# Performance work log

Hardware: AMD Instinct MI355X
Metric: run time of the kernel (lower is better)

The kernel has to match this reference:

```python
import jax, jax.numpy as jnp
import numpy as np

N_NODES = 100000
N_EDGES = 2000000
N_GRAPHS = 2000
IN_DIM = 7
EDGE_DIM = 4
HID = 32
N_CLASSES = 2
NEG_SLOPE = 0.2
BN_EPS = 1e-5


def setup_inputs() -> dict:
    key = jax.random.key(0)
    ks = jax.random.split(key, 16)
    x = jax.random.normal(ks[0], (N_NODES, IN_DIM), dtype=jnp.float32)
    edge_index = jax.random.randint(ks[1], (2, N_EDGES), 0, N_NODES, dtype=jnp.int64)
    batch = jnp.sort(jax.random.randint(ks[2], (N_NODES,), 0, N_GRAPHS, dtype=jnp.int64))
    edge_attr = jax.random.normal(ks[3], (N_EDGES, EDGE_DIM), dtype=jnp.float32)
    s = 0.1
    W0 = jax.random.normal(ks[4], (IN_DIM, HID), dtype=jnp.float32) * s
    W12 = jax.random.normal(ks[5], (2, HID, HID), dtype=jnp.float32) * s
    att_src = jax.random.normal(ks[6], (3, HID), dtype=jnp.float32) * s
    att_dst = jax.random.normal(ks[7], (3, HID), dtype=jnp.float32) * s
    lin_edge = jax.random.normal(ks[8], (3, EDGE_DIM, HID), dtype=jnp.float32) * s
    att_edge = jax.random.normal(ks[9], (3, HID), dtype=jnp.float32) * s
    bias = jnp.zeros((3, HID), dtype=jnp.float32)
    bn_gamma = jnp.ones((3, HID), dtype=jnp.float32)
    bn_beta = jnp.zeros((3, HID), dtype=jnp.float32)
    fc_W = jax.random.normal(ks[10], (HID, N_CLASSES), dtype=jnp.float32) * s
    fc_b = jnp.zeros((N_CLASSES,), dtype=jnp.float32)
    return dict(x=x, edge_index=edge_index, batch=batch, edge_attr=edge_attr,
                W0=W0, W12=W12, att_src=att_src, att_dst=att_dst,
                lin_edge=lin_edge, att_edge=att_edge, bias=bias,
                bn_gamma=bn_gamma, bn_beta=bn_beta, fc_W=fc_W, fc_b=fc_b)


def gat_layer(x, src, dst, edge_attr, W, a_src, a_dst, We, a_edge, b):
    # PyG GATConv, heads=1, add_self_loops=False: edge_attr conditions attention only.
    N = x.shape[0]
    h = x @ W                                   # [N, H]
    e = edge_attr @ We                          # [E, H]
    score = ((h * a_src).sum(-1)[src]
             + (h * a_dst).sum(-1)[dst]
             + (e * a_edge).sum(-1))            # [E]
    score = jax.nn.leaky_relu(score, NEG_SLOPE)
    m = jax.ops.segment_max(score, dst, num_segments=N)
    w = jnp.exp(score - m[dst])
    denom = jax.ops.segment_sum(w, dst, num_segments=N)
    alpha = w / (denom[dst] + 1e-16)            # segment softmax over incoming edges
    out = jax.ops.segment_sum(h[src] * alpha[:, None], dst, num_segments=N)
    return out + b


def batchnorm(x, gamma, beta):
    mu = x.mean(axis=0)
    var = ((x - mu) ** 2).mean(axis=0)          # biased var, as torch BN normalization
    return (x - mu) * jax.lax.rsqrt(var + BN_EPS) * gamma + beta


def reference(x, edge_index, batch, edge_attr, W0, W12, att_src, att_dst,
              lin_edge, att_edge, bias, bn_gamma, bn_beta, fc_W, fc_b):
    src, dst = edge_index[0], edge_index[1]
    Ws = [W0, W12[0], W12[1]]
    h = x
    for l in range(3):
        h = gat_layer(h, src, dst, edge_attr, Ws[l], att_src[l], att_dst[l],
                      lin_edge[l], att_edge[l], bias[l])
        h = batchnorm(h, bn_gamma[l], bn_beta[l])
        h = jax.nn.relu(h)
    node_embs = h
    graph_emb = jax.ops.segment_sum(node_embs, batch, num_segments=N_GRAPHS)
    out = graph_emb @ fc_W + fc_b
    return (out, node_embs, graph_emb)
```

## Files before the change

kernel.cpp:

```cpp
#include <hip/hip_runtime.h>
#include <hip/hip_bf16.h>
#include <math.h>

#define N_NODES   100000
#define N_EDGES   2000000
#define N_GRAPHS  2000
#define IN_DIM    7
#define EDGE_DIM  4
#define HID       32
#define N_CLASSES 2
#define NEG_SLOPE 0.2f
#define BN_EPS    1e-5f
#define SCAN_B    1024

__global__ void k_ce_all(const float* __restrict__ lin_edge, const float* __restrict__ att_edge,
                         float* __restrict__ ce3, float* __restrict__ gsum3,
                         float* __restrict__ gsq3) {
    int t = threadIdx.x;
    if (t < 12) {
        int l = t >> 2, d = t & 3;
        float s = 0.f;
        for (int k = 0; k < HID; ++k)
            s += lin_edge[(size_t)l * EDGE_DIM * HID + d * HID + k] * att_edge[l * HID + k];
        ce3[t] = s;
    }
    if (t < 3 * HID) { gsum3[t] = 0.f; gsq3[t] = 0.f; }
}

__global__ void k_hist(const int* __restrict__ dst, int* __restrict__ deg) {
    int e = blockIdx.x * blockDim.x + threadIdx.x;
    if (e < N_EDGES) atomicAdd(deg + dst[e], 1);
}

__global__ void k_scan1(const int* __restrict__ deg, int* __restrict__ offs,
                        int* __restrict__ bsum) {
    __shared__ int wsum[16];
    int t = threadIdx.x, lane = t & 63, w = t >> 6;
    int i = blockIdx.x * SCAN_B + t;
    int v = (i < N_NODES) ? deg[i] : 0;
    int x = v;
#pragma unroll
    for (int o = 1; o < 64; o <<= 1) { int y = __shfl_up(x, o, 64); if (lane >= o) x += y; }
    if (lane == 63) wsum[w] = x;
    __syncthreads();
    if (t < 16) {
        int s = wsum[t];
#pragma unroll
        for (int o = 1; o < 16; o <<= 1) { int y = __shfl_up(s, o, 16); if (t >= o) s += y; }
        wsum[t] = s;
    }
    __syncthreads();
    int excl = (w ? wsum[w - 1] : 0) + x - v;
    if (i < N_NODES) offs[i] = excl;
    if (t == 0) bsum[blockIdx.x] = wsum[15];
}

__global__ void k_scan2(int* __restrict__ bsum, int nb) {
    __shared__ int w0;
    int t = threadIdx.x, lane = t & 63, w = t >> 6;
    int v = (t < nb) ? bsum[t] : 0;
    int x = v;
#pragma unroll
    for (int o = 1; o < 64; o <<= 1) { int y = __shfl_up(x, o, 64); if (lane >= o) x += y; }
    if (w == 0 && lane == 63) w0 = x;
    __syncthreads();
    int excl = x - v + (w ? w0 : 0);
    if (t < nb) bsum[t] = excl;
}

__global__ void k_scan3(int* __restrict__ offs, const int* __restrict__ bsum,
                        int* __restrict__ cursor) {
    int i = blockIdx.x * SCAN_B + threadIdx.x;
    if (i < N_NODES) {
        int o = offs[i] + bsum[blockIdx.x];
        offs[i] = o;
        cursor[i] = o;
    }
}

__global__ void k_scatter(const int* __restrict__ src, const int* __restrict__ dst,
                          const float4* __restrict__ eattr, const float* __restrict__ ce3,
                          int* __restrict__ cursor, int4* __restrict__ pack) {
    int e = blockIdx.x * blockDim.x + threadIdx.x;
    if (e >= N_EDGES) return;
    float4 ea = eattr[e];
    float e0 = ea.x * ce3[0] + ea.y * ce3[1] + ea.z * ce3[2] + ea.w * ce3[3];
    float e1 = ea.x * ce3[4] + ea.y * ce3[5] + ea.z * ce3[6] + ea.w * ce3[7];
    float e2 = ea.x * ce3[8] + ea.y * ce3[9] + ea.z * ce3[10] + ea.w * ce3[11];
    int d = dst[e];
    int pos = atomicAdd(cursor + d, 1);
    pack[pos] = make_int4(src[e], __float_as_int(e0), __float_as_int(e1), __float_as_int(e2));
}

template <int INDIM, bool BN>
__global__ void k_linear(const float* __restrict__ in, const float* __restrict__ W,
                         const float* __restrict__ a_src, const float* __restrict__ a_dst,
                         const float* __restrict__ gsum, const float* __restrict__ gsq,
                         const float* __restrict__ gamma, const float* __restrict__ beta,
                         __hip_bfloat16* __restrict__ h, float* __restrict__ asrc,
                         float* __restrict__ adst) {
    __shared__ float Ws[INDIM * HID];
    for (int i = threadIdx.x; i < INDIM * HID; i += blockDim.x) Ws[i] = W[i];
    __syncthreads();
    int g = threadIdx.x >> 5, k = threadIdx.x & 31;
    int n = blockIdx.x * 8 + g;
    if (n >= N_NODES) return;
    float xv;
    if (BN) {
        const float invN = 1.f / (float)N_NODES;
        float mu = gsum[k] * invN;
        float var = gsq[k] * invN - mu * mu;
        var = fmaxf(var, 0.f);
        float scl = rsqrtf(var + BN_EPS) * gamma[k];
        float v = (in[(size_t)n * INDIM + k] - mu) * scl + beta[k];
        xv = fmaxf(v, 0.f);
    } else {
        xv = (k < INDIM) ? in[(size_t)n * INDIM + k] : 0.f;
    }
    float acc = 0.f;
#pragma unroll
    for (int d = 0; d < INDIM; ++d) acc += __shfl(xv, d, 32) * Ws[d * HID + k];
    h[(size_t)n * HID + k] = __float2bfloat16(acc);
    float vs = acc * a_src[k];
    float vd = acc * a_dst[k];
#pragma unroll
    for (int m = 16; m > 0; m >>= 1) {
        vs += __shfl_xor(vs, m, 32);
        vd += __shfl_xor(vd, m, 32);
    }
    if (k == 0) { asrc[n] = vs; adst[n] = vd; }
}

template <int L>
__global__ void k_aggr(const int4* __restrict__ pack, const int* __restrict__ offs,
                       const int* __restrict__ endp, const __hip_bfloat16* __restrict__ hb,
                       const float* __restrict__ asrc, const float* __restrict__ adst,
                       const float* __restrict__ bias, float* __restrict__ out,
                       float* __restrict__ gsum, float* __restrict__ gsq) {
    __shared__ float ssum[HID], ssq[HID];
    if (threadIdx.x < HID) { ssum[threadIdx.x] = 0.f; ssq[threadIdx.x] = 0.f; }
    __syncthreads();
    int g = threadIdx.x >> 5, k = threadIdx.x & 31;
    int n = blockIdx.x * 8 + g;
    if (n < N_NODES) {
        int pbeg = offs[n], en = endp[n];
        float ad = adst[n];
        float den = 0.f, a = 0.f;
        for (int p = pbeg; p < en; p += 8) {
            int4 pk[8];
            float as[8], hh[8];
#pragma unroll
            for (int j = 0; j < 8; ++j) {
                int q = p + j;
                q = q < en ? q : en - 1;
                pk[j] = pack[q];
            }
#pragma unroll
            for (int j = 0; j < 8; ++j) as[j] = asrc[pk[j].x];
#pragma unroll
            for (int j = 0; j < 8; ++j)
                hh[j] = __bfloat162float(hb[(size_t)pk[j].x * HID + k]);
#pragma unroll
            for (int j = 0; j < 8; ++j) {
                float edot = __int_as_float(L == 0 ? pk[j].y : (L == 1 ? pk[j].z : pk[j].w));
                float sc = as[j] + ad + edot;
                sc = sc > 0.f ? sc : NEG_SLOPE * sc;
                float w = (p + j < en) ? __expf(sc) : 0.f;
                den += w;
                a = fmaf(w, hh[j], a);
            }
        }
        float v = a / (den + 1e-16f) + bias[k];
        out[(size_t)n * HID + k] = v;
        atomicAdd(&ssum[k], v);
        atomicAdd(&ssq[k], v * v);
    }
    __syncthreads();
    if (threadIdx.x < HID) {
        atomicAdd(gsum + threadIdx.x, ssum[threadIdx.x]);
        atomicAdd(gsq + threadIdx.x, ssq[threadIdx.x]);
    }
}

__global__ void k_bn_relu_pool(const float* __restrict__ acc, const float* __restrict__ gsum,
                               const float* __restrict__ gsq, const float* __restrict__ gamma,
                               const float* __restrict__ beta, const int* __restrict__ batch,
                               float* __restrict__ nemb, float* __restrict__ gemb) {
    int g = threadIdx.x >> 5, k = threadIdx.x & 31;
    int n = blockIdx.x * 8 + g;
    if (n >= N_NODES) return;
    const float invN = 1.f / (float)N_NODES;
    float mu = gsum[k] * invN;
    float var = gsq[k] * invN - mu * mu;
    var = fmaxf(var, 0.f);
    float scl = rsqrtf(var + BN_EPS) * gamma[k];
    float v = (acc[(size_t)n * HID + k] - mu) * scl + beta[k];
    v = fmaxf(v, 0.f);
    nemb[(size_t)n * HID + k] = v;
    atomicAdd(gemb + (size_t)batch[n] * HID + k, v);
}

__global__ void k_fc(const float* __restrict__ gemb, const float* __restrict__ W,
                     const float* __restrict__ b, float* __restrict__ out) {
    int g = blockIdx.x * blockDim.x + threadIdx.x;
    if (g >= N_GRAPHS) return;
    float a0 = b[0], a1 = b[1];
    for (int k = 0; k < HID; ++k) {
        float v = gemb[(size_t)g * HID + k];
        a0 += v * W[k * 2 + 0];
        a1 += v * W[k * 2 + 1];
    }
    out[g * 2 + 0] = a0;
    out[g * 2 + 1] = a1;
}

extern "C" void kernel_launch(void* const* d_in, const int* in_sizes, int n_in,
                              void* d_out, int out_size, void* d_ws, size_t ws_size,
                              hipStream_t stream) {
    const float* x        = (const float*)d_in[0];
    const int*   ei       = (const int*)d_in[1];
    const int*   batch    = (const int*)d_in[2];
    const float* eattr    = (const float*)d_in[3];
    const float* W0       = (const float*)d_in[4];
    const float* W12      = (const float*)d_in[5];
    const float* att_src  = (const float*)d_in[6];
    const float* att_dst  = (const float*)d_in[7];
    const float* lin_edge = (const float*)d_in[8];
    const float* att_edge = (const float*)d_in[9];
    const float* bias     = (const float*)d_in[10];
    const float* bn_gamma = (const float*)d_in[11];
    const float* bn_beta  = (const float*)d_in[12];
    const float* fc_W     = (const float*)d_in[13];
    const float* fc_b     = (const float*)d_in[14];

    const int* srcA = ei;
    const int* dstA = ei + N_EDGES;

    float* out       = (float*)d_out;
    float* node_embs = out + N_GRAPHS * N_CLASSES;
    float* graph_emb = node_embs + (size_t)N_NODES * HID;

    char* ws = (char*)d_ws;
    size_t off = 0;
    auto alloc = [&](size_t bytes) { char* p = ws + off; off += (bytes + 255) & ~(size_t)255; return p; };
    __hip_bfloat16* hT = (__hip_bfloat16*)alloc((size_t)N_NODES * HID * 2);
    float* A0    = (float*)alloc((size_t)N_NODES * HID * 4);
    float* A1    = (float*)alloc((size_t)N_NODES * HID * 4);
    int4*  pack  = (int4*)alloc((size_t)N_EDGES * 16);
    int*   deg   = (int*)alloc((size_t)N_NODES * 4);
    int*   offs  = (int*)alloc((size_t)N_NODES * 4);
    int*   cursor= (int*)alloc((size_t)N_NODES * 4);
    int*   bsum  = (int*)alloc(128 * 4);
    float* asrc  = (float*)alloc((size_t)N_NODES * 4);
    float* adst  = (float*)alloc((size_t)N_NODES * 4);
    float* ce3   = (float*)alloc(12 * 4);
    float* gsum3 = (float*)alloc(3 * HID * 4);
    float* gsq3  = (float*)alloc(3 * HID * 4);
    (void)ws_size;

    const int nodeBlocks8 = (N_NODES + 7) / 8;
    const int edgeBlocks  = (N_EDGES + 255) / 256;
    const int scanBlocks  = (N_NODES + SCAN_B - 1) / SCAN_B;

    hipMemsetAsync(deg, 0, (size_t)N_NODES * 4, stream);
    k_ce_all<<<1, 128, 0, stream>>>(lin_edge, att_edge, ce3, gsum3, gsq3);
    k_hist<<<edgeBlocks, 256, 0, stream>>>(dstA, deg);
    k_scan1<<<scanBlocks, SCAN_B, 0, stream>>>(deg, offs, bsum);
    k_scan2<<<1, 128, 0, stream>>>(bsum, scanBlocks);
    k_scan3<<<scanBlocks, SCAN_B, 0, stream>>>(offs, bsum, cursor);
    k_scatter<<<edgeBlocks, 256, 0, stream>>>(srcA, dstA, (const float4*)eattr, ce3, cursor, pack);

    k_linear<IN_DIM, false><<<nodeBlocks8, 256, 0, stream>>>(
        x, W0, att_src, att_dst, nullptr, nullptr, nullptr, nullptr, hT, asrc, adst);
    k_aggr<0><<<nodeBlocks8, 256, 0, stream>>>(pack, offs, cursor, hT, asrc, adst,
                                               bias, A0, gsum3, gsq3);
    k_linear<HID, true><<<nodeBlocks8, 256, 0, stream>>>(
        A0, W12, att_src + HID, att_dst + HID, gsum3, gsq3, bn_gamma, bn_beta, hT, asrc, adst);
    k_aggr<1><<<nodeBlocks8, 256, 0, stream>>>(pack, offs, cursor, hT, asrc, adst,
                                               bias + HID, A1, gsum3 + HID, gsq3 + HID);
    k_linear<HID, true><<<nodeBlocks8, 256, 0, stream>>>(
        A1, W12 + HID * HID, att_src + 2 * HID, att_dst + 2 * HID,
        gsum3 + HID, gsq3 + HID, bn_gamma + HID, bn_beta + HID, hT, asrc, adst);
    k_aggr<2><<<nodeBlocks8, 256, 0, stream>>>(pack, offs, cursor, hT, asrc, adst,
                                               bias + 2 * HID, A0, gsum3 + 2 * HID, gsq3 + 2 * HID);

    hipMemsetAsync(graph_emb, 0, (size_t)N_GRAPHS * HID * 4, stream);
    k_bn_relu_pool<<<nodeBlocks8, 256, 0, stream>>>(A0, gsum3 + 2 * HID, gsq3 + 2 * HID,
                                                    bn_gamma + 2 * HID, bn_beta + 2 * HID,
                                                    batch, node_embs, graph_emb);
    k_fc<<<(N_GRAPHS + 255) / 256, 256, 0, stream>>>(graph_emb, fc_W, fc_b, out);
}
```

Baseline: 952.2 us.

## Split edge-weight computation into per-edge kernel and vectorise aggregation by bf16 pairs

```diff
diff --git a/kernel.cpp b/kernel.cpp
--- a/kernel.cpp
+++ b/kernel.cpp
@@ -12,6 +12,11 @@
 #define NEG_SLOPE 0.2f
 #define BN_EPS    1e-5f
 #define SCAN_B    1024
+
+__device__ __forceinline__ unsigned bfbits(float f) {
+    unsigned u = __float_as_uint(f);
+    return (u + 0x7FFFu + ((u >> 16) & 1u)) >> 16;
+}
 
 __global__ void k_ce_all(const float* __restrict__ lin_edge, const float* __restrict__ att_edge,
                          float* __restrict__ ce3, float* __restrict__ gsum3,
@@ -89,7 +94,9 @@
     float e2 = ea.x * ce3[8] + ea.y * ce3[9] + ea.z * ce3[10] + ea.w * ce3[11];
     int d = dst[e];
     int pos = atomicAdd(cursor + d, 1);
-    pack[pos] = make_int4(src[e], __float_as_int(e0), __float_as_int(e1), __float_as_int(e2));
+    pack[pos] = make_int4(src[e], d,
+                          (int)(bfbits(e0) | (bfbits(e1) << 16)),
+                          (int)bfbits(e2));
 }
 
 template <int INDIM, bool BN>
@@ -132,48 +139,72 @@
 }
 
 template <int L>
-__global__ void k_aggr(const int4* __restrict__ pack, const int* __restrict__ offs,
+__global__ void k_edgew(const int4* __restrict__ pack, const float* __restrict__ asrc,
+                        const float* __restrict__ adst, int2* __restrict__ rec) {
+    int e = blockIdx.x * blockDim.x + threadIdx.x;
+    if (e >= N_EDGES) return;
+    int4 pk = pack[e];
+    unsigned z = (unsigned)pk.z;
+    float edot;
+    if (L == 0)      edot = __uint_as_float((z & 0xFFFFu) << 16);
+    else if (L == 1) edot = __uint_as_float(z & 0xFFFF0000u);
+    else             edot = __uint_as_float(((unsigned)pk.w & 0xFFFFu) << 16);
+    float sc = asrc[pk.x] + adst[pk.y] + edot;
+    sc = fmaxf(sc, NEG_SLOPE * sc);
+    float w = __expf(sc);
+    rec[e] = make_int2(pk.x, __float_as_int(w));
+}
+
+__global__ void k_aggr(const int2* __restrict__ rec, const int* __restrict__ offs,
                        const int* __restrict__ endp, const __hip_bfloat16* __restrict__ hb,
-                       const float* __restrict__ asrc, const float* __restrict__ adst,
                        const float* __restrict__ bias, float* __restrict__ out,
                        float* __restrict__ gsum, float* __restrict__ gsq) {
     __shared__ float ssum[HID], ssq[HID];
     if (threadIdx.x < HID) { ssum[threadIdx.x] = 0.f; ssq[threadIdx.x] = 0.f; }
     __syncthreads();
-    int g = threadIdx.x >> 5, k = threadIdx.x & 31;
+    int g = threadIdx.x >> 5;
+    int lane = threadIdx.x & 31;
+    int sub = lane >> 4;
+    int c2 = lane & 15;
     int n = blockIdx.x * 8 + g;
     if (n < N_NODES) {
         int pbeg = offs[n], en = endp[n];
-        float ad = adst[n];
-        float den = 0.f, a = 0.f;
+        float den = 0.f, a0 = 0.f, a1 = 0.f;
         for (int p = pbeg; p < en; p += 8) {
-            int4 pk[8];
-            float as[8], hh[8];
-#pragma unroll
-            for (int j = 0; j < 8; ++j) {
-                int q = p + j;
+            int2 rc[4];
+            unsigned hw[4];
+#pragma unroll
+            for (int m = 0; m < 4; ++m) {
+                int q = p + 2 * m + sub;
                 q = q < en ? q : en - 1;
-                pk[j] = pack[q];
+                rc[m] = rec[q];
             }
 #pragma unroll
-            for (int j = 0; j < 8; ++j) as[j] = asrc[pk[j].x];
-#pragma unroll
-            for (int j = 0; j < 8; ++j)
-                hh[j] = __bfloat162float(hb[(size_t)pk[j].x * HID + k]);
-#pragma unroll
-            for (int j = 0; j < 8; ++j) {
-                float edot = __int_as_float(L == 0 ? pk[j].y : (L == 1 ? pk[j].z : pk[j].w));
-                float sc = as[j] + ad + edot;
-                sc = sc > 0.f ? sc : NEG_SLOPE * sc;
-                float w = (p + j < en) ? __expf(sc) : 0.f;
+            for (int m = 0; m < 4; ++m)
+                hw[m] = *(const unsigned*)(hb + (size_t)rc[m].x * HID + 2 * c2);
+#pragma unroll
+            for (int m = 0; m < 4; ++m) {
+                float w = (p + 2 * m + sub < en) ? __int_as_float(rc[m].y) : 0.f;
                 den += w;
-                a = fmaf(w, hh[j], a);
+                float lo = __uint_as_float((hw[m] & 0xFFFFu) << 16);
+                float hi = __uint_as_float(hw[m] & 0xFFFF0000u);
+                a0 = fmaf(w, lo, a0);
+                a1 = fmaf(w, hi, a1);
             }
         }
-        float v = a / (den + 1e-16f) + bias[k];
-        out[(size_t)n * HID + k] = v;
-        atomicAdd(&ssum[k], v);
-        atomicAdd(&ssq[k], v * v);
+        den += __shfl_xor(den, 16, 32);
+        a0  += __shfl_xor(a0, 16, 32);
+        a1  += __shfl_xor(a1, 16, 32);
+        if (sub == 0) {
+            float inv = 1.f / (den + 1e-16f);
+            float v0 = a0 * inv + bias[2 * c2];
+            float v1 = a1 * inv + bias[2 * c2 + 1];
+            *(float2*)(out + (size_t)n * HID + 2 * c2) = make_float2(v0, v1);
+            atomicAdd(&ssum[2 * c2], v0);
+            atomicAdd(&ssum[2 * c2 + 1], v1);
+            atomicAdd(&ssq[2 * c2], v0 * v0);
+            atomicAdd(&ssq[2 * c2 + 1], v1 * v1);
+        }
     }
     __syncthreads();
     if (threadIdx.x < HID) {
@@ -244,9 +275,9 @@
     size_t off = 0;
     auto alloc = [&](size_t bytes) { char* p = ws + off; off += (bytes + 255) & ~(size_t)255; return p; };
     __hip_bfloat16* hT = (__hip_bfloat16*)alloc((size_t)N_NODES * HID * 2);
-    float* A0    = (float*)alloc((size_t)N_NODES * HID * 4);
-    float* A1    = (float*)alloc((size_t)N_NODES * HID * 4);
+    float* A     = (float*)alloc((size_t)N_NODES * HID * 4);
     int4*  pack  = (int4*)alloc((size_t)N_EDGES * 16);
+    int2*  rec   = (int2*)alloc((size_t)N_EDGES * 8);
     int*   deg   = (int*)alloc((size_t)N_NODES * 4);
     int*   offs  = (int*)alloc((size_t)N_NODES * 4);
     int*   cursor= (int*)alloc((size_t)N_NODES * 4);
@@ -272,20 +303,22 @@
 
     k_linear<IN_DIM, false><<<nodeBlocks8, 256, 0, stream>>>(
         x, W0, att_src, att_dst, nullptr, nullptr, nullptr, nullptr, hT, asrc, adst);
-    k_aggr<0><<<nodeBlocks8, 256, 0, stream>>>(pack, offs, cursor, hT, asrc, adst,
-                                               bias, A0, gsum3, gsq3);
+    k_edgew<0><<<edgeBlocks, 256, 0, stream>>>(pack, asrc, adst, rec);
+    k_aggr<<<nodeBlocks8, 256, 0, stream>>>(rec, offs, cursor, hT, bias, A, gsum3, gsq3);
     k_linear<HID, true><<<nodeBlocks8, 256, 0, stream>>>(
-        A0, W12, att_src + HID, att_dst + HID, gsum3, gsq3, bn_gamma, bn_beta, hT, asrc, adst);
-    k_aggr<1><<<nodeBlocks8, 256, 0, stream>>>(pack, offs, cursor, hT, asrc, adst,
-                                               bias + HID, A1, gsum3 + HID, gsq3 + HID);
+        A, W12, att_src + HID, att_dst + HID, gsum3, gsq3, bn_gamma, bn_beta, hT, asrc, adst);
+    k_edgew<1><<<edgeBlocks, 256, 0, stream>>>(pack, asrc, adst, rec);
+    k_aggr<<<nodeBlocks8, 256, 0, stream>>>(rec, offs, cursor, hT, bias + HID, A,
+                                            gsum3 + HID, gsq3 + HID);
     k_linear<HID, true><<<nodeBlocks8, 256, 0, stream>>>(
-        A1, W12 + HID * HID, att_src + 2 * HID, att_dst + 2 * HID,
+        A, W12 + HID * HID, att_src + 2 * HID, att_dst + 2 * HID,
         gsum3 + HID, gsq3 + HID, bn_gamma + HID, bn_beta + HID, hT, asrc, adst);
-    k_aggr<2><<<nodeBlocks8, 256, 0, stream>>>(pack, offs, cursor, hT, asrc, adst,
-                                               bias + 2 * HID, A0, gsum3 + 2 * HID, gsq3 + 2 * HID);
+    k_edgew<2><<<edgeBlocks, 256, 0, stream>>>(pack, asrc, adst, rec);
+    k_aggr<<<nodeBlocks8, 256, 0, stream>>>(rec, offs, cursor, hT, bias + 2 * HID, A,
+                                            gsum3 + 2 * HID, gsq3 + 2 * HID);
 
     hipMemsetAsync(graph_emb, 0, (size_t)N_GRAPHS * HID * 4, stream);
-    k_bn_relu_pool<<<nodeBlocks8, 256, 0, stream>>>(A0, gsum3 + 2 * HID, gsq3 + 2 * HID,
+    k_bn_relu_pool<<<nodeBlocks8, 256, 0, stream>>>(A, gsum3 + 2 * HID, gsq3 + 2 * HID,
                                                     bn_gamma + 2 * HID, bn_beta + 2 * HID,
                                                     batch, node_embs, graph_emb);
     k_fc<<<(N_GRAPHS + 255) / 256, 256, 0, stream>>>(graph_emb, fc_W, fc_b, out);
```

After: 987.7 us. +3.7%, slower.
